# Kernel optimization log

Hardware: AMD Instinct MI355X
Metric: run time of the kernel (lower is better)

## Reference

```python
import jax, jax.numpy as jnp
import numpy as np

EPS = 1e-5   # BatchNorm eps
OUT = 256    # resize target


def _crop_bounds(img):
    # A row/col is 'whitespace' iff all its values are identical (len(unique)==1),
    # i.e. min == max along that axis. This fuses the torch while-loops into reductions.
    col_var = img.min(axis=0) != img.max(axis=0)   # [W] True where column non-constant
    row_var = img.min(axis=1) != img.max(axis=1)   # [H]
    H, W = img.shape
    any_c = jnp.any(col_var)
    any_r = jnp.any(row_var)
    left = jnp.where(any_c, jnp.argmax(col_var), 0)
    right = jnp.where(any_c, W - 1 - jnp.argmax(col_var[::-1]), W - 1)
    top = jnp.where(any_r, jnp.argmax(row_var), 0)
    bottom = jnp.where(any_r, H - 1 - jnp.argmax(row_var[::-1]), H - 1)
    return top, bottom, left, right


def _crop_resize_bilinear(img, top, bottom, left, right, out=OUT):
    # Fused crop + bilinear resize (align_corners=False, torchvision-style),
    # avoids data-dependent output shapes: sample 256x256 grid inside the crop box.
    def axis_coords(lo, hi):
        size = (hi - lo + 1).astype(jnp.float32)
        c = lo.astype(jnp.float32) + (jnp.arange(out, dtype=jnp.float32) + 0.5) * size / out - 0.5
        c0 = jnp.floor(c)
        w = c - c0
        i0 = jnp.clip(c0, lo, hi).astype(jnp.int32)
        i1 = jnp.clip(c0 + 1.0, lo, hi).astype(jnp.int32)
        return i0, i1, w
    y0, y1, wy = axis_coords(top, bottom)
    x0, x1, wx = axis_coords(left, right)
    g = lambda yi, xi: img[yi[:, None], xi[None, :]]   # [256,256] gather
    top_row = g(y0, x0) * (1.0 - wx)[None, :] + g(y0, x1) * wx[None, :]
    bot_row = g(y1, x0) * (1.0 - wx)[None, :] + g(y1, x1) * wx[None, :]
    return top_row * (1.0 - wy)[:, None] + bot_row * wy[:, None]


DN = ('NCHW', 'OIHW', 'NCHW')


def _conv_block(x, w, b, gamma, beta, mean, var):
    # l2l ConvBlock with max_pool=False: Conv2d(k=3, stride=2, pad=1) -> BN(eval) -> ReLU
    x = jax.lax.conv_general_dilated(x, w, (2, 2), [(1, 1), (1, 1)], dimension_numbers=DN)
    x = x + b[None, :, None, None]
    scale = gamma / jnp.sqrt(var + EPS)
    x = (x - mean[None, :, None, None]) * scale[None, :, None, None] + beta[None, :, None, None]
    return jax.nn.relu(x)


def _forward(image, conv0_w, conv0_b, convs_w, convs_b, bn_gamma, bn_beta, bn_mean, bn_var, head_w, head_b):
    t, b, l, r = _crop_bounds(image)
    resized = _crop_resize_bilinear(image, t, b, l, r)            # [256,256]
    im = (255.0 - resized)[None, None]                             # [1,1,256,256]
    ones_k = jnp.ones((1, 1, 3, 3), im.dtype)
    dil = jax.lax.conv_general_dilated(im, ones_k, (1, 1), 'SAME', rhs_dilation=(2, 2), dimension_numbers=DN)
    x = 255.0 - jnp.clip(dil, 0.0, 255.0)                          # [1,1,256,256]
    x = _conv_block(x, conv0_w, conv0_b, bn_gamma[0], bn_beta[0], bn_mean[0], bn_var[0])
    for i in range(4):  # fixed small layer count
        x = _conv_block(x, convs_w[i], convs_b[i], bn_gamma[i + 1], bn_beta[i + 1], bn_mean[i + 1], bn_var[i + 1])
    feat = x.mean(axis=(2, 3))                                     # [1,64]
    logits = feat @ head_w.T + head_b                              # [1,2]
    return logits


def setup_inputs() -> dict:
    key = jax.random.key(0)
    ks = jax.random.split(key, 12)
    H = W = 8192
    hidden, ways = 64, 2
    return {
        'image': jax.random.normal(ks[0], (H, W), dtype=jnp.float32),
        'conv0_w': jax.random.normal(ks[1], (hidden, 1, 3, 3), dtype=jnp.float32) * 0.1,
        'conv0_b': jax.random.normal(ks[2], (hidden,), dtype=jnp.float32) * 0.1,
        'convs_w': jax.random.normal(ks[3], (4, hidden, hidden, 3, 3), dtype=jnp.float32) * 0.05,
        'convs_b': jax.random.normal(ks[4], (4, hidden), dtype=jnp.float32) * 0.1,
        'bn_gamma': jnp.ones((5, hidden), dtype=jnp.float32) + 0.1 * jax.random.normal(ks[5], (5, hidden)),
        'bn_beta': jax.random.normal(ks[6], (5, hidden), dtype=jnp.float32) * 0.1,
        'bn_mean': jax.random.normal(ks[7], (5, hidden), dtype=jnp.float32) * 0.1,
        'bn_var': jax.random.uniform(ks[8], (5, hidden), dtype=jnp.float32, minval=0.5, maxval=1.5),
        'head_w': jax.random.normal(ks[9], (ways, hidden), dtype=jnp.float32) * 0.1,
        'head_b': jax.random.normal(ks[10], (ways,), dtype=jnp.float32) * 0.1,
    }


def reference(image, conv0_w, conv0_b, convs_w, convs_b, bn_gamma, bn_beta, bn_mean, bn_var, head_w, head_b):
    logits = _forward(image, conv0_w, conv0_b, convs_w, convs_b, bn_gamma, bn_beta, bn_mean, bn_var, head_w, head_b)
    return jnp.argmax(logits, axis=1)  # predicted_label, shape [1]
```

## Files before the change

kernel.cpp:

```cpp
#include <hip/hip_runtime.h>
#include <hip/hip_bf16.h>


#define IMG_H 8192
#define IMG_W 8192
#define EPS 1e-5f

__device__ __forceinline__ int scan_nonconst(const float* __restrict__ base,
                                             int n, long stride, int* sflag) {
  const int tid = threadIdx.x;
  const float ref = base[0];
  for (int start = 0; start < n; start += 1024) {
    if (tid == 0) *sflag = 0;
    __syncthreads();
    int f = 0;
#pragma unroll
    for (int u = 0; u < 4; ++u) {
      const int k = start + u * 256 + tid;
      if (k < n && base[(long)k * stride] != ref) f = 1;
    }
    if (f) *sflag = 1;
    __syncthreads();
    if (*sflag) return 1;
  }
  return 0;
}

__global__ __launch_bounds__(256) void crop_bounds_k(
    const float* __restrict__ img, int* __restrict__ bounds) {
  __shared__ int sflag;
  const int dir = blockIdx.x;
  if (dir == 0) {
    for (int r = 0; r < IMG_H; ++r)
      if (scan_nonconst(img + (long)r * IMG_W, IMG_W, 1, &sflag)) {
        if (threadIdx.x == 0) bounds[0] = r;
        return;
      }
    if (threadIdx.x == 0) bounds[0] = 0;
  } else if (dir == 1) {
    for (int r = IMG_H - 1; r >= 0; --r)
      if (scan_nonconst(img + (long)r * IMG_W, IMG_W, 1, &sflag)) {
        if (threadIdx.x == 0) bounds[1] = r;
        return;
      }
    if (threadIdx.x == 0) bounds[1] = IMG_H - 1;
  } else if (dir == 2) {
    for (int c = 0; c < IMG_W; ++c)
      if (scan_nonconst(img + c, IMG_H, IMG_W, &sflag)) {
        if (threadIdx.x == 0) bounds[2] = c;
        return;
      }
    if (threadIdx.x == 0) bounds[2] = 0;
  } else {
    for (int c = IMG_W - 1; c >= 0; --c)
      if (scan_nonconst(img + c, IMG_H, IMG_W, &sflag)) {
        if (threadIdx.x == 0) bounds[3] = c;
        return;
      }
    if (threadIdx.x == 0) bounds[3] = IMG_W - 1;
  }
}

__global__ __launch_bounds__(256) void resize_invert_k(
    const float* __restrict__ img, const int* __restrict__ bounds,
    float* __restrict__ im) {
  const int i = blockIdx.x;
  const int j = threadIdx.x;
  const int t = bounds[0], b = bounds[1], l = bounds[2], r = bounds[3];
  const float sy = (float)(b - t + 1);
  const float sx = (float)(r - l + 1);
  const float cy = (float)t + ((float)i + 0.5f) * sy / 256.0f - 0.5f;
  const float cx = (float)l + ((float)j + 0.5f) * sx / 256.0f - 0.5f;
  const float cy0 = floorf(cy), cx0 = floorf(cx);
  const float wy = cy - cy0, wx = cx - cx0;
  const int y0 = (int)fminf(fmaxf(cy0, (float)t), (float)b);
  const int y1 = (int)fminf(fmaxf(cy0 + 1.0f, (float)t), (float)b);
  const int x0 = (int)fminf(fmaxf(cx0, (float)l), (float)r);
  const int x1 = (int)fminf(fmaxf(cx0 + 1.0f, (float)l), (float)r);
  const float v00 = img[(long)y0 * IMG_W + x0];
  const float v01 = img[(long)y0 * IMG_W + x1];
  const float v10 = img[(long)y1 * IMG_W + x0];
  const float v11 = img[(long)y1 * IMG_W + x1];
  const float top_row = v00 * (1.0f - wx) + v01 * wx;
  const float bot_row = v10 * (1.0f - wx) + v11 * wx;
  const float res = top_row * (1.0f - wy) + bot_row * wy;
  im[i * 256 + j] = 255.0f - res;
}

__global__ __launch_bounds__(256) void dilate_invert_k(
    const float* __restrict__ im, float* __restrict__ out) {
  const int i = blockIdx.x;
  const int j = threadIdx.x;
  float s = 0.0f;
#pragma unroll
  for (int dy = -2; dy <= 2; dy += 2) {
    const int y = i + dy;
    if ((unsigned)y >= 256u) continue;
#pragma unroll
    for (int dx = -2; dx <= 2; dx += 2) {
      const int x = j + dx;
      if ((unsigned)x >= 256u) continue;
      s += im[y * 256 + x];
    }
  }
  out[i * 256 + j] = 255.0f - fminf(fmaxf(s, 0.0f), 255.0f);
}

__global__ __launch_bounds__(256) void conv_bn_relu_k(
    const float* __restrict__ in, const float* __restrict__ wt,
    const float* __restrict__ bias, const float* __restrict__ gamma,
    const float* __restrict__ beta, const float* __restrict__ mean,
    const float* __restrict__ var, float* __restrict__ out,
    int IC, int IH, int IW, int OH, int OW) {
  __shared__ float wl[8 * 64 * 9];
  const int ocg = blockIdx.z * 8;
  const int nW = 8 * IC * 9;
  for (int idx = threadIdx.x; idx < nW; idx += 256)
    wl[idx] = wt[(long)ocg * IC * 9 + idx];
  __syncthreads();

  const int ox = blockIdx.x * 16 + (threadIdx.x & 15);
  const int oy = blockIdx.y * 16 + (threadIdx.x >> 4);
  if (ox >= OW || oy >= OH) return;

  float acc[8];
#pragma unroll
  for (int o = 0; o < 8; ++o) acc[o] = 0.0f;

  const int iy0 = 2 * oy - 1;
  const int ix0 = 2 * ox - 1;
  for (int ic = 0; ic < IC; ++ic) {
    const float* __restrict__ ip = in + (long)ic * IH * IW;
    const float* __restrict__ wp = wl + ic * 9;
#pragma unroll
    for (int ky = 0; ky < 3; ++ky) {
      const int iy = iy0 + ky;
      if ((unsigned)iy >= (unsigned)IH) continue;
#pragma unroll
      for (int kx = 0; kx < 3; ++kx) {
        const int ix = ix0 + kx;
        if ((unsigned)ix >= (unsigned)IW) continue;
        const float v = ip[(long)iy * IW + ix];
        const int t = ky * 3 + kx;
#pragma unroll
        for (int o = 0; o < 8; ++o)
          acc[o] = fmaf(v, wp[o * IC * 9 + t], acc[o]);
      }
    }
  }

#pragma unroll
  for (int o = 0; o < 8; ++o) {
    const int oc = ocg + o;
    const float s = gamma[oc] / sqrtf(var[oc] + EPS);
    const float v = (acc[o] + bias[oc] - mean[oc]) * s + beta[oc];
    out[((long)oc * OH + oy) * OW + ox] = fmaxf(v, 0.0f);
  }
}

__global__ __launch_bounds__(64) void head_argmax_k(
    const float* __restrict__ x, const float* __restrict__ hw,
    const float* __restrict__ hb, float* __restrict__ out) {
  const int c = threadIdx.x;
  float s = 0.0f;
#pragma unroll
  for (int k = 0; k < 64; ++k) s += x[c * 64 + k];
  const float feat = s * (1.0f / 64.0f);
  float p0 = feat * hw[c];
  float p1 = feat * hw[64 + c];
#pragma unroll
  for (int off = 32; off > 0; off >>= 1) {
    p0 += __shfl_down(p0, off);
    p1 += __shfl_down(p1, off);
  }
  if (c == 0) {
    const float l0 = p0 + hb[0];
    const float l1 = p1 + hb[1];
    out[0] = (l1 > l0) ? 1.0f : 0.0f;
  }
}

extern "C" void kernel_launch(void* const* d_in, const int* in_sizes, int n_in,
                              void* d_out, int out_size, void* d_ws,
                              size_t ws_size, hipStream_t stream) {
  const float* image   = (const float*)d_in[0];
  const float* conv0_w = (const float*)d_in[1];
  const float* conv0_b = (const float*)d_in[2];
  const float* convs_w = (const float*)d_in[3];
  const float* convs_b = (const float*)d_in[4];
  const float* bn_g    = (const float*)d_in[5];
  const float* bn_b    = (const float*)d_in[6];
  const float* bn_m    = (const float*)d_in[7];
  const float* bn_v    = (const float*)d_in[8];
  const float* head_w  = (const float*)d_in[9];
  const float* head_b  = (const float*)d_in[10];

  float* W = (float*)d_ws;
  int* bounds = (int*)d_ws;
  float* im = W + 16;
  float* x1 = im + 65536;
  float* c0 = x1 + 65536;
  float* c1 = c0 + 1048576;
  float* c2 = c1 + 262144;
  float* c3 = c2 + 65536;
  float* c4 = c3 + 16384;

  crop_bounds_k<<<4, 256, 0, stream>>>(image, bounds);
  resize_invert_k<<<256, 256, 0, stream>>>(image, bounds, im);
  dilate_invert_k<<<256, 256, 0, stream>>>(im, x1);

  conv_bn_relu_k<<<dim3(8, 8, 8), 256, 0, stream>>>(
      x1, conv0_w, conv0_b, bn_g, bn_b, bn_m, bn_v, c0, 1, 256, 256, 128, 128);
  conv_bn_relu_k<<<dim3(4, 4, 8), 256, 0, stream>>>(
      c0, convs_w + 0 * 36864, convs_b + 0 * 64, bn_g + 64, bn_b + 64,
      bn_m + 64, bn_v + 64, c1, 64, 128, 128, 64, 64);
  conv_bn_relu_k<<<dim3(2, 2, 8), 256, 0, stream>>>(
      c1, convs_w + 1 * 36864, convs_b + 1 * 64, bn_g + 128, bn_b + 128,
      bn_m + 128, bn_v + 128, c2, 64, 64, 64, 32, 32);
  conv_bn_relu_k<<<dim3(1, 1, 8), 256, 0, stream>>>(
      c2, convs_w + 2 * 36864, convs_b + 2 * 64, bn_g + 192, bn_b + 192,
      bn_m + 192, bn_v + 192, c3, 64, 32, 32, 16, 16);
  conv_bn_relu_k<<<dim3(1, 1, 8), 256, 0, stream>>>(
      c3, convs_w + 3 * 36864, convs_b + 3 * 64, bn_g + 256, bn_b + 256,
      bn_m + 256, bn_v + 256, c4, 64, 16, 16, 8, 8);

  head_argmax_k<<<1, 64, 0, stream>>>(c4, head_w, head_b, (float*)d_out);
}
```

Measured before the change: 701.4 us.

## Fuse resize with dilation and spread small conv layers across more blocks

```diff
diff --git a/kernel.cpp b/kernel.cpp
--- a/kernel.cpp
+++ b/kernel.cpp
@@ -61,60 +61,69 @@
   }
 }
 
-__global__ __launch_bounds__(256) void resize_invert_k(
+__global__ __launch_bounds__(256) void resize_dilate_k(
     const float* __restrict__ img, const int* __restrict__ bounds,
-    float* __restrict__ im) {
+    float* __restrict__ out) {
+  __shared__ float s[3][256];
   const int i = blockIdx.x;
   const int j = threadIdx.x;
-  const int t = bounds[0], b = bounds[1], l = bounds[2], r = bounds[3];
-  const float sy = (float)(b - t + 1);
-  const float sx = (float)(r - l + 1);
-  const float cy = (float)t + ((float)i + 0.5f) * sy / 256.0f - 0.5f;
-  const float cx = (float)l + ((float)j + 0.5f) * sx / 256.0f - 0.5f;
-  const float cy0 = floorf(cy), cx0 = floorf(cx);
-  const float wy = cy - cy0, wx = cx - cx0;
-  const int y0 = (int)fminf(fmaxf(cy0, (float)t), (float)b);
-  const int y1 = (int)fminf(fmaxf(cy0 + 1.0f, (float)t), (float)b);
-  const int x0 = (int)fminf(fmaxf(cx0, (float)l), (float)r);
-  const int x1 = (int)fminf(fmaxf(cx0 + 1.0f, (float)l), (float)r);
-  const float v00 = img[(long)y0 * IMG_W + x0];
-  const float v01 = img[(long)y0 * IMG_W + x1];
-  const float v10 = img[(long)y1 * IMG_W + x0];
-  const float v11 = img[(long)y1 * IMG_W + x1];
-  const float top_row = v00 * (1.0f - wx) + v01 * wx;
-  const float bot_row = v10 * (1.0f - wx) + v11 * wx;
-  const float res = top_row * (1.0f - wy) + bot_row * wy;
-  im[i * 256 + j] = 255.0f - res;
-}
-
-__global__ __launch_bounds__(256) void dilate_invert_k(
-    const float* __restrict__ im, float* __restrict__ out) {
-  const int i = blockIdx.x;
-  const int j = threadIdx.x;
-  float s = 0.0f;
-#pragma unroll
-  for (int dy = -2; dy <= 2; dy += 2) {
-    const int y = i + dy;
+  const int tb = bounds[0], bb = bounds[1], lb = bounds[2], rb = bounds[3];
+  const float sy = (float)(bb - tb + 1);
+  const float sx = (float)(rb - lb + 1);
+
+  const float cx = (float)lb + ((float)j + 0.5f) * sx / 256.0f - 0.5f;
+  const float cx0 = floorf(cx);
+  const float wx = cx - cx0;
+  const int x0 = (int)fminf(fmaxf(cx0, (float)lb), (float)rb);
+  const int x1 = (int)fminf(fmaxf(cx0 + 1.0f, (float)lb), (float)rb);
+
+#pragma unroll
+  for (int k = 0; k < 3; ++k) {
+    const int row = i + 2 * (k - 1);
+    float v = 0.0f;
+    if ((unsigned)row < 256u) {
+      const float cy = (float)tb + ((float)row + 0.5f) * sy / 256.0f - 0.5f;
+      const float cy0 = floorf(cy);
+      const float wy = cy - cy0;
+      const int y0 = (int)fminf(fmaxf(cy0, (float)tb), (float)bb);
+      const int y1 = (int)fminf(fmaxf(cy0 + 1.0f, (float)tb), (float)bb);
+      const float v00 = img[(long)y0 * IMG_W + x0];
+      const float v01 = img[(long)y0 * IMG_W + x1];
+      const float v10 = img[(long)y1 * IMG_W + x0];
+      const float v11 = img[(long)y1 * IMG_W + x1];
+      const float tr = v00 * (1.0f - wx) + v01 * wx;
+      const float br = v10 * (1.0f - wx) + v11 * wx;
+      v = 255.0f - (tr * (1.0f - wy) + br * wy);
+    }
+    s[k][j] = v;
+  }
+  __syncthreads();
+
+  float sum = 0.0f;
+#pragma unroll
+  for (int k = 0; k < 3; ++k) {
+    const int y = i + 2 * (k - 1);
     if ((unsigned)y >= 256u) continue;
 #pragma unroll
     for (int dx = -2; dx <= 2; dx += 2) {
       const int x = j + dx;
       if ((unsigned)x >= 256u) continue;
-      s += im[y * 256 + x];
-    }
-  }
-  out[i * 256 + j] = 255.0f - fminf(fmaxf(s, 0.0f), 255.0f);
-}
-
+      sum += s[k][x];
+    }
+  }
+  out[i * 256 + j] = 255.0f - fminf(fmaxf(sum, 0.0f), 255.0f);
+}
+
+template <int OCP>
 __global__ __launch_bounds__(256) void conv_bn_relu_k(
     const float* __restrict__ in, const float* __restrict__ wt,
     const float* __restrict__ bias, const float* __restrict__ gamma,
     const float* __restrict__ beta, const float* __restrict__ mean,
     const float* __restrict__ var, float* __restrict__ out,
     int IC, int IH, int IW, int OH, int OW) {
-  __shared__ float wl[8 * 64 * 9];
-  const int ocg = blockIdx.z * 8;
-  const int nW = 8 * IC * 9;
+  __shared__ float wl[OCP * 64 * 9];
+  const int ocg = blockIdx.z * OCP;
+  const int nW = OCP * IC * 9;
   for (int idx = threadIdx.x; idx < nW; idx += 256)
     wl[idx] = wt[(long)ocg * IC * 9 + idx];
   __syncthreads();
@@ -123,9 +132,9 @@
   const int oy = blockIdx.y * 16 + (threadIdx.x >> 4);
   if (ox >= OW || oy >= OH) return;
 
-  float acc[8];
-#pragma unroll
-  for (int o = 0; o < 8; ++o) acc[o] = 0.0f;
+  float acc[OCP];
+#pragma unroll
+  for (int o = 0; o < OCP; ++o) acc[o] = 0.0f;
 
   const int iy0 = 2 * oy - 1;
   const int ix0 = 2 * ox - 1;
@@ -143,19 +152,55 @@
         const float v = ip[(long)iy * IW + ix];
         const int t = ky * 3 + kx;
 #pragma unroll
-        for (int o = 0; o < 8; ++o)
+        for (int o = 0; o < OCP; ++o)
           acc[o] = fmaf(v, wp[o * IC * 9 + t], acc[o]);
       }
     }
   }
 
 #pragma unroll
-  for (int o = 0; o < 8; ++o) {
+  for (int o = 0; o < OCP; ++o) {
     const int oc = ocg + o;
     const float s = gamma[oc] / sqrtf(var[oc] + EPS);
     const float v = (acc[o] + bias[oc] - mean[oc]) * s + beta[oc];
     out[((long)oc * OH + oy) * OW + ox] = fmaxf(v, 0.0f);
   }
+}
+
+__global__ __launch_bounds__(64) void conv4_k(
+    const float* __restrict__ in, const float* __restrict__ wt,
+    const float* __restrict__ bias, const float* __restrict__ gamma,
+    const float* __restrict__ beta, const float* __restrict__ mean,
+    const float* __restrict__ var, float* __restrict__ out) {
+  __shared__ float wl[64 * 9];
+  const int oc = blockIdx.x;
+  for (int idx = threadIdx.x; idx < 576; idx += 64)
+    wl[idx] = wt[oc * 576 + idx];
+  __syncthreads();
+
+  const int ox = threadIdx.x & 7;
+  const int oy = threadIdx.x >> 3;
+  const int iy0 = 2 * oy - 1;
+  const int ix0 = 2 * ox - 1;
+  float acc = 0.0f;
+  for (int ic = 0; ic < 64; ++ic) {
+    const float* __restrict__ ip = in + ic * 256;
+    const float* __restrict__ wp = wl + ic * 9;
+#pragma unroll
+    for (int ky = 0; ky < 3; ++ky) {
+      const int iy = iy0 + ky;
+      if ((unsigned)iy >= 16u) continue;
+#pragma unroll
+      for (int kx = 0; kx < 3; ++kx) {
+        const int ix = ix0 + kx;
+        if ((unsigned)ix >= 16u) continue;
+        acc = fmaf(ip[iy * 16 + ix], wp[ky * 3 + kx], acc);
+      }
+    }
+  }
+  const float s = gamma[oc] / sqrtf(var[oc] + EPS);
+  const float v = (acc + bias[oc] - mean[oc]) * s + beta[oc];
+  out[oc * 64 + threadIdx.x] = fmaxf(v, 0.0f);
 }
 
 __global__ __launch_bounds__(64) void head_argmax_k(
@@ -197,8 +242,7 @@
 
   float* W = (float*)d_ws;
   int* bounds = (int*)d_ws;
-  float* im = W + 16;
-  float* x1 = im + 65536;
+  float* x1 = W + 16;
   float* c0 = x1 + 65536;
   float* c1 = c0 + 1048576;
   float* c2 = c1 + 262144;
@@ -206,23 +250,22 @@
   float* c4 = c3 + 16384;
 
   crop_bounds_k<<<4, 256, 0, stream>>>(image, bounds);
-  resize_invert_k<<<256, 256, 0, stream>>>(image, bounds, im);
-  dilate_invert_k<<<256, 256, 0, stream>>>(im, x1);
-
-  conv_bn_relu_k<<<dim3(8, 8, 8), 256, 0, stream>>>(
+  resize_dilate_k<<<256, 256, 0, stream>>>(image, bounds, x1);
+
+  conv_bn_relu_k<8><<<dim3(8, 8, 8), 256, 0, stream>>>(
       x1, conv0_w, conv0_b, bn_g, bn_b, bn_m, bn_v, c0, 1, 256, 256, 128, 128);
-  conv_bn_relu_k<<<dim3(4, 4, 8), 256, 0, stream>>>(
+  conv_bn_relu_k<4><<<dim3(4, 4, 16), 256, 0, stream>>>(
       c0, convs_w + 0 * 36864, convs_b + 0 * 64, bn_g + 64, bn_b + 64,
       bn_m + 64, bn_v + 64, c1, 64, 128, 128, 64, 64);
-  conv_bn_relu_k<<<dim3(2, 2, 8), 256, 0, stream>>>(
+  conv_bn_relu_k<2><<<dim3(2, 2, 32), 256, 0, stream>>>(
       c1, convs_w + 1 * 36864, convs_b + 1 * 64, bn_g + 128, bn_b + 128,
       bn_m + 128, bn_v + 128, c2, 64, 64, 64, 32, 32);
-  conv_bn_relu_k<<<dim3(1, 1, 8), 256, 0, stream>>>(
+  conv_bn_relu_k<1><<<dim3(1, 1, 64), 256, 0, stream>>>(
       c2, convs_w + 2 * 36864, convs_b + 2 * 64, bn_g + 192, bn_b + 192,
       bn_m + 192, bn_v + 192, c3, 64, 32, 32, 16, 16);
-  conv_bn_relu_k<<<dim3(1, 1, 8), 256, 0, stream>>>(
+  conv4_k<<<64, 64, 0, stream>>>(
       c3, convs_w + 3 * 36864, convs_b + 3 * 64, bn_g + 256, bn_b + 256,
-      bn_m + 256, bn_v + 256, c4, 64, 16, 16, 8, 8);
+      bn_m + 256, bn_v + 256, c4);
 
   head_argmax_k<<<1, 64, 0, stream>>>(c4, head_w, head_b, (float*)d_out);
 }
```

Result: faster. 629.8 us (-10.2%).
